# Optimization experiments

Measured on AMD Instinct MI355X. Metric: run time of the kernel, lower is better.

Reference implementation:

```python
import jax, jax.numpy as jnp
import numpy as np

B, NR, NF, NH, NFH, D, HID = 32, 32, 128, 64, 64, 32, 256


def setup_inputs() -> dict:
    key = jax.random.key(0)
    ks = jax.random.split(key, 16)

    def w(k, o, i):
        return (jax.random.normal(k, (o, i), jnp.float32) / np.sqrt(i)).astype(jnp.float32)

    inp = {
        "robot": jax.random.normal(ks[0], (B, NR, D), jnp.float32),
        "frontier": jax.random.normal(ks[1], (B, NF, D), jnp.float32),
        "robot_history": jax.random.normal(ks[2], (B, NH, D), jnp.float32),
        "frontier_history": jax.random.normal(ks[3], (B, NFH, D), jnp.float32),
        "robot_frontier": jax.random.uniform(ks[4], (B, NR, NF), jnp.float32),
        "robot_past": jax.random.uniform(ks[5], (B, NR, NH), jnp.float32),
        "frontier_past": jax.random.uniform(ks[6], (B, NF, NFH), jnp.float32),
        # parameters (torch Linear convention: weight [out, in])
        "Wq": w(ks[7], D, D), "bq": jnp.zeros(D, jnp.float32),
        "Wk": w(ks[8], D, D), "bk": jnp.zeros(D, jnp.float32),
        "Wv": w(ks[9], D, D), "bv": jnp.zeros(D, jnp.float32),
        "Wn1": w(ks[10], HID, 2 * D), "bn1": jnp.zeros(HID, jnp.float32),
        "Wn2": w(ks[11], D, HID), "bn2": jnp.zeros(D, jnp.float32),
        "We1": w(ks[12], HID, 2 * D + 1), "be1": jnp.zeros(HID, jnp.float32),
        "We2": w(ks[13], 1, HID), "be2": jnp.zeros(1, jnp.float32),
    }
    return inp


def reference(robot, frontier, robot_history, frontier_history, robot_frontier,
              robot_past, frontier_past, Wq, bq, Wk, bk, Wv, bv,
              Wn1, bn1, Wn2, bn2, We1, be1, We2, be2):
    def lin(x, W, b):
        return x @ W.T + b

    def nmlp(h):
        return lin(jax.nn.relu(lin(h, Wn1, bn1)), Wn2, bn2)

    def emlp(h):
        return lin(jax.nn.relu(lin(h, We1, be1)), We2, be2)

    def intra(x):  # x: [b, n, D]
        q, k, v = lin(x, Wq, bq), lin(x, Wk, bk), lin(x, Wv, bv)
        e = jax.nn.softmax(jnp.einsum('bnd,bmd->bnm', q, k), axis=-1)
        agg = jnp.einsum('bnm,bmd->bnd', e, v)
        return x + nmlp(jnp.concatenate([x, agg], axis=-1))

    def inter(x, y, dis):  # x: [b,Nx,D], y: [b,Ny,D], dis: [b,Nx,Ny]
        xq, yk, yv = lin(x, Wq, bq), lin(y, Wk, bk), lin(y, Wv, bv)
        b, Nx, _ = x.shape
        Ny = y.shape[1]
        r_i = jnp.broadcast_to(xq[:, :, None, :], (b, Nx, Ny, D))
        f_j = jnp.broadcast_to(yk[:, None, :, :], (b, Nx, Ny, D))
        edge_input = jnp.concatenate([r_i, f_j, dis[..., None]], axis=-1)  # [b,Nx,Ny,65]
        score = emlp(edge_input)[..., 0]                                   # [b,Nx,Ny]
        e = jax.nn.softmax(score, axis=-1)
        agg = jnp.einsum('bnm,bmd->bnd', e, yv)
        x = x + nmlp(jnp.concatenate([x, agg], axis=-1))
        return e, x

    robot = intra(robot)
    frontier = intra(frontier)           # == per-sample intra on [1,Nf,D]
    robot_history = intra(robot_history)
    frontier_history = intra(frontier_history)
    _, robot = inter(robot, robot_history, robot_past)
    _, new_frontier = inter(frontier, frontier_history, frontier_past)
    edge, robot = inter(robot, new_frontier, robot_frontier)
    # original returns the intra-transformed frontier (split_frontier), not new_frontier
    return (robot, frontier, robot_history, frontier_history, edge)
```

## Files before the change

### kernel.cpp

```cpp
#include <hip/hip_runtime.h>

#define BATCH 32
#define NRr 32
#define NFf 128
#define NHh 64
#define NFHh 64
#define TI 4

__device__ __forceinline__ float dot4(float4 a, float4 b) {
    return fmaf(a.x, b.x, fmaf(a.y, b.y, fmaf(a.z, b.z, a.w * b.w)));
}

__global__ __launch_bounds__(256) void intra_kernel(
    const float* __restrict__ robot, const float* __restrict__ frontier,
    const float* __restrict__ rhist, const float* __restrict__ fhist,
    const float* __restrict__ Wq, const float* __restrict__ bq,
    const float* __restrict__ Wk, const float* __restrict__ bk,
    const float* __restrict__ Wv, const float* __restrict__ bv,
    const float* __restrict__ Wn1, const float* __restrict__ bn1,
    const float* __restrict__ Wn2, const float* __restrict__ bn2,
    float* __restrict__ o_robot, float* __restrict__ o_frontier,
    float* __restrict__ o_rh, float* __restrict__ o_fh)
{
    __shared__ __align__(16) float sXc[1024];
    __shared__ __align__(16) float sQ[1024];
    __shared__ __align__(16) float sAgg[1024];
    __shared__ __align__(16) float sS[4096];
    __shared__ __align__(16) float sKT[4128];
    __shared__ __align__(16) float sVT[8192];

    const int blk = blockIdx.x, tid = threadIdx.x;
    const float* xin; float* xout; int N, lgN, b, chunk;
    if (blk < 32)       { xin=robot;    xout=o_robot;    N=32;  lgN=5; b=blk;          chunk=0; }
    else if (blk < 160) { xin=frontier; xout=o_frontier; N=128; lgN=7; b=(blk-32)>>2;  chunk=(blk-32)&3; }
    else if (blk < 224) { xin=rhist;    xout=o_rh;       N=64;  lgN=6; b=(blk-160)>>1; chunk=(blk-160)&1; }
    else                { xin=fhist;    xout=o_fh;       N=64;  lgN=6; b=(blk-224)>>1; chunk=(blk-224)&1; }

    const float* xb = xin + (size_t)b * N * 32;
    const int r0 = chunk << 5;
    const int d = tid & 31;

    {
        int idx = tid;
        #pragma unroll
        for (int it = 0; it < 4; ++it, idx += 256)
            sXc[idx] = xb[(r0 << 5) + idx];
    }

    {
        const float4* wk4 = (const float4*)(Wk + (d << 5));
        const float4* wv4 = (const float4*)(Wv + (d << 5));
        float4 wk[8], wv[8];
        #pragma unroll
        for (int k = 0; k < 8; ++k) { wk[k] = wk4[k]; wv[k] = wv4[k]; }
        const float bkd = bk[d], bvd = bv[d];
        for (int idx = tid; idx < (N << 5); idx += 256) {
            int j = idx >> 5;
            const float4* xr = (const float4*)(xb + (j << 5));
            float aK = bkd, aV = bvd;
            #pragma unroll
            for (int k = 0; k < 8; ++k) {
                float4 xv = xr[k];
                aK += dot4(wk[k], xv);
                aV += dot4(wv[k], xv);
            }
            sKT[d * 129 + j] = aK;
            sVT[(j << 5) + d] = aV;
        }
    }
    __syncthreads();

    {
        const float4* wq4 = (const float4*)(Wq + (d << 5));
        float4 wq[8];
        #pragma unroll
        for (int k = 0; k < 8; ++k) wq[k] = wq4[k];
        const float bqd = bq[d];
        int idx = tid;
        #pragma unroll
        for (int it = 0; it < 4; ++it, idx += 256) {
            int r = idx >> 5;
            const float4* xr = (const float4*)(sXc + (r << 5));
            float a = bqd;
            #pragma unroll
            for (int k = 0; k < 8; ++k) a += dot4(wq[k], xr[k]);
            sQ[idx] = a;
        }
    }
    __syncthreads();

    for (int idx = tid; idx < (N << 5); idx += 256) {
        int r = idx >> lgN, j = idx & (N - 1);
        const float* qr = sQ + (r << 5);
        float a = 0.f;
        #pragma unroll
        for (int e = 0; e < 32; ++e) a = fmaf(qr[e], sKT[e * 129 + j], a);
        sS[idx] = a;
    }
    __syncthreads();

    {
        int r = tid >> 3, l = tid & 7;
        float* row = sS + (r << lgN);
        float m = -1e30f;
        for (int j = l; j < N; j += 8) m = fmaxf(m, row[j]);
        m = fmaxf(m, __shfl_xor(m, 4));
        m = fmaxf(m, __shfl_xor(m, 2));
        m = fmaxf(m, __shfl_xor(m, 1));
        float s = 0.f;
        for (int j = l; j < N; j += 8) { float ev = __expf(row[j] - m); row[j] = ev; s += ev; }
        s += __shfl_xor(s, 4); s += __shfl_xor(s, 2); s += __shfl_xor(s, 1);
        float inv = 1.0f / s;
        for (int j = l; j < N; j += 8) row[j] *= inv;
    }
    __syncthreads();

    {
        int idx = tid;
        #pragma unroll
        for (int it = 0; it < 4; ++it, idx += 256) {
            int r = idx >> 5;
            const float* er = sS + (r << lgN);
            float a = 0.f;
            for (int j = 0; j < N; ++j) a = fmaf(er[j], sVT[(j << 5) + d], a);
            sAgg[idx] = a;
        }
    }
    __syncthreads();

    float* sT = sVT;
    {
        const float4* w14 = (const float4*)(Wn1 + (tid << 6));
        float4 w1r[16];
        #pragma unroll
        for (int k = 0; k < 16; ++k) w1r[k] = w14[k];
        const float b1 = bn1[tid];
        for (int r = 0; r < 32; ++r) {
            const float4* xr = (const float4*)(sXc + (r << 5));
            const float4* ar = (const float4*)(sAgg + (r << 5));
            float a = b1;
            #pragma unroll
            for (int k = 0; k < 8; ++k) a += dot4(w1r[k], xr[k]);
            #pragma unroll
            for (int k = 0; k < 8; ++k) a += dot4(w1r[8 + k], ar[k]);
            sT[(r << 8) + tid] = fmaxf(a, 0.f);
        }
    }
    __syncthreads();

    {
        const int rg = tid >> 5;
        float acc[4] = {0.f, 0.f, 0.f, 0.f};
        #pragma unroll
        for (int hc = 0; hc < 4; ++hc) {
            const float4* w24 = (const float4*)(Wn2 + (d << 8) + (hc << 6));
            float4 w2r[16];
            #pragma unroll
            for (int k = 0; k < 16; ++k) w2r[k] = w24[k];
            #pragma unroll
            for (int p = 0; p < 4; ++p) {
                int r = rg + (p << 3);
                const float4* tr = (const float4*)(sT + (r << 8) + (hc << 6));
                float a = 0.f;
                #pragma unroll
                for (int k = 0; k < 16; ++k) a += dot4(w2r[k], tr[k]);
                acc[p] += a;
            }
        }
        const float b2 = bn2[d];
        #pragma unroll
        for (int p = 0; p < 4; ++p) {
            int r = rg + (p << 3);
            xout[((size_t)b * N << 5) + ((r0 + r) << 5) + d] = sXc[(r << 5) + d] + b2 + acc[p];
        }
    }
}

__global__ __launch_bounds__(256) void pre_y_kernel(
    const float* __restrict__ yA, int NyA, float* __restrict__ wOutA, float* __restrict__ yvOutA, int nBlkA,
    const float* __restrict__ yB, int NyB, float* __restrict__ wOutB, float* __restrict__ yvOutB,
    const float* __restrict__ Wk, const float* __restrict__ bk,
    const float* __restrict__ Wv, const float* __restrict__ bv,
    const float* __restrict__ We1)
{
    __shared__ __align__(16) float sY[256], sK[256];
    const int blk = blockIdx.x, tid = threadIdx.x;
    const float* y; int Ny; float* wOut; float* yvOut; int idx;
    if (blk < nBlkA) { y=yA; Ny=NyA; wOut=wOutA; yvOut=yvOutA; idx=blk; }
    else             { y=yB; Ny=NyB; wOut=wOutB; yvOut=yvOutB; idx=blk-nBlkA; }
    const int chunks = Ny >> 3;
    const int b = idx / chunks, j0 = (idx - b * chunks) << 3;

    sY[tid] = y[((size_t)(b * Ny + j0)) * 32 + tid];
    __syncthreads();

    {
        int jl = tid >> 5, dd = tid & 31;
        const float4* wk4 = (const float4*)(Wk + (dd << 5));
        const float4* wv4 = (const float4*)(Wv + (dd << 5));
        const float4* yr = (const float4*)(sY + (jl << 5));
        float aK = bk[dd], aV = bv[dd];
        #pragma unroll
        for (int k = 0; k < 8; ++k) {
            float4 yv4 = yr[k];
            aK += dot4(wk4[k], yv4);
            aV += dot4(wv4[k], yv4);
        }
        sK[(jl << 5) + dd] = aK;
        yvOut[((size_t)(b * Ny + j0 + jl)) * 32 + dd] = aV;
    }
    __syncthreads();

    {
        const float* w1 = We1 + tid * 65 + 32;
        float acc[8] = {0,0,0,0,0,0,0,0};
        #pragma unroll
        for (int e = 0; e < 32; ++e) {
            float we = w1[e];
            #pragma unroll
            for (int jl = 0; jl < 8; ++jl)
                acc[jl] = fmaf(we, sK[(jl << 5) + e], acc[jl]);
        }
        float* wbase = wOut + (((size_t)b * 64 + (tid >> 2)) * Ny + j0) * 4 + (tid & 3);
        #pragma unroll
        for (int jl = 0; jl < 8; ++jl)
            wbase[jl << 2] = acc[jl];
    }
}

__global__ __launch_bounds__(256) void inter_main_kernel(
    const float* __restrict__ xA, int NxA, const float* __restrict__ wA, const float* __restrict__ yvA,
    int NyA, const float* __restrict__ disA, float* __restrict__ outA, float* __restrict__ eA, int nBlkA,
    const float* __restrict__ xB, int NxB, const float* __restrict__ wB, const float* __restrict__ yvB,
    int NyB, const float* __restrict__ disB, float* __restrict__ outB, float* __restrict__ eB,
    const float* __restrict__ Wq, const float* __restrict__ bq,
    const float* __restrict__ We1, const float* __restrict__ be1,
    const float* __restrict__ We2,
    const float* __restrict__ Wn1, const float* __restrict__ bn1,
    const float* __restrict__ Wn2, const float* __restrict__ bn2)
{
    __shared__ __align__(16) float smem[9088];
    float* sX   = smem;
    float* sQ   = smem + 128;
    float* sAgg = smem + 256;
    float* sDis = smem + 384;
    float* sC   = smem + 896;
    float* sW2  = smem + 1152;
    float* sS   = smem + 1408;
    float* sUT  = smem + 1920;
    float* sPR  = smem + 2944;
    float* sYV  = smem + 4992;

    const int blk = blockIdx.x, tid = threadIdx.x;
    const float* x; int Nx; const float* w; const float* yv; int Ny;
    const float* dis; float* outp; float* ep; int idx;
    if (blk < nBlkA) { x=xA; Nx=NxA; w=wA; yv=yvA; Ny=NyA; dis=disA; outp=outA; ep=eA; idx=blk; }
    else             { x=xB; Nx=NxB; w=wB; yv=yvB; Ny=NyB; dis=disB; outp=outB; ep=eB; idx=blk-nBlkA; }
    const int lgNy = (Ny == 128) ? 7 : 6;
    const int tiles = Nx >> 2;
    const int b = idx / tiles, i0 = (idx - b * tiles) << 2;
    const float* xrow = x + ((size_t)(b * Nx + i0)) * 32;

    if (tid < 128) sX[tid] = xrow[tid];
    if (tid < Ny) {
        int il = tid >> (lgNy - 2), jq = tid & ((Ny >> 2) - 1);
        ((float4*)sDis)[(il << 5) + jq] =
            ((const float4*)(dis + ((size_t)(b * Nx + i0 + il)) * Ny))[jq];
    }
    {
        const float4* yv4 = (const float4*)(yv + ((size_t)(b * Ny) << 5));
        for (int k = tid; k < (Ny << 3); k += 256)
            ((float4*)sYV)[k] = yv4[k];
    }
    __syncthreads();

    if (tid < 128) {
        int il = tid >> 5, dd = tid & 31;
        const float4* wq4 = (const float4*)(Wq + (dd << 5));
        const float4* xr = (const float4*)(sX + (il << 5));
        float a = bq[dd];
        #pragma unroll
        for (int k = 0; k < 8; ++k) a += dot4(wq4[k], xr[k]);
        sQ[tid] = a;
    }
    __syncthreads();

    {
        const float* w1 = We1 + tid * 65;
        const float b1 = be1[tid];
        float acc[TI];
        #pragma unroll
        for (int il = 0; il < TI; ++il) acc[il] = b1;
        #pragma unroll
        for (int e = 0; e < 32; ++e) {
            float we = w1[e];
            #pragma unroll
            for (int il = 0; il < TI; ++il)
                acc[il] = fmaf(we, sQ[(il << 5) + e], acc[il]);
        }
        #pragma unroll
        for (int il = 0; il < TI; ++il) sUT[(il << 8) + tid] = acc[il];
        sC[tid] = w1[64];
        sW2[tid] = We2[tid];
    }
    __syncthreads();

    const int wv = tid >> 6, lane = tid & 63;
    {
        const int hc0 = wv << 4;
        const float4* wT4 = (const float4*)w + (size_t)(b * 64) * Ny;
        const float4* c4p = (const float4*)sC;
        const float4* p4p = (const float4*)sW2;
        if (Ny == 64) {
            float dv[TI];
            #pragma unroll
            for (int il = 0; il < TI; ++il) dv[il] = sDis[(il << 7) + lane];
            float acc[TI] = {0.f, 0.f, 0.f, 0.f};
            #pragma unroll
            for (int t = 0; t < 16; ++t) {
                int hc = hc0 + t;
                float4 w4 = wT4[((size_t)hc << 6) + lane];
                float4 c4 = c4p[hc], p4 = p4p[hc];
                #pragma unroll
                for (int il = 0; il < TI; ++il) {
                    float4 u4 = ((const float4*)(sUT + (il << 8)))[hc];
                    acc[il] = fmaf(p4.x, fmaxf(fmaf(c4.x, dv[il], u4.x + w4.x), 0.f), acc[il]);
                    acc[il] = fmaf(p4.y, fmaxf(fmaf(c4.y, dv[il], u4.y + w4.y), 0.f), acc[il]);
                    acc[il] = fmaf(p4.z, fmaxf(fmaf(c4.z, dv[il], u4.z + w4.z), 0.f), acc[il]);
                    acc[il] = fmaf(p4.w, fmaxf(fmaf(c4.w, dv[il], u4.w + w4.w), 0.f), acc[il]);
                }
            }
            #pragma unroll
            for (int il = 0; il < TI; ++il)
                sPR[(wv << 9) + (il << 7) + lane] = acc[il];
        } else {
            float dv0[TI], dv1[TI];
            #pragma unroll
            for (int il = 0; il < TI; ++il) {
                dv0[il] = sDis[(il << 7) + lane];
                dv1[il] = sDis[(il << 7) + 64 + lane];
            }
            float acc0[TI] = {0.f, 0.f, 0.f, 0.f};
            float acc1[TI] = {0.f, 0.f, 0.f, 0.f};
            #pragma unroll
            for (int t = 0; t < 16; ++t) {
                int hc = hc0 + t;
                float4 wa = wT4[((size_t)hc << 7) + lane];
                float4 wb = wT4[((size_t)hc << 7) + 64 + lane];
                float4 c4 = c4p[hc], p4 = p4p[hc];
                #pragma unroll
                for (int il = 0; il < TI; ++il) {
                    float4 u4 = ((const float4*)(sUT + (il << 8)))[hc];
                    acc0[il] = fmaf(p4.x, fmaxf(fmaf(c4.x, dv0[il], u4.x + wa.x), 0.f), acc0[il]);
                    acc0[il] = fmaf(p4.y, fmaxf(fmaf(c4.y, dv0[il], u4.y + wa.y), 0.f), acc0[il]);
                    acc0[il] = fmaf(p4.z, fmaxf(fmaf(c4.z, dv0[il], u4.z + wa.z), 0.f), acc0[il]);
                    acc0[il] = fmaf(p4.w, fmaxf(fmaf(c4.w, dv0[il], u4.w + wa.w), 0.f), acc0[il]);
                    acc1[il] = fmaf(p4.x, fmaxf(fmaf(c4.x, dv1[il], u4.x + wb.x), 0.f), acc1[il]);
                    acc1[il] = fmaf(p4.y, fmaxf(fmaf(c4.y, dv1[il], u4.y + wb.y), 0.f), acc1[il]);
                    acc1[il] = fmaf(p4.z, fmaxf(fmaf(c4.z, dv1[il], u4.z + wb.z), 0.f), acc1[il]);
                    acc1[il] = fmaf(p4.w, fmaxf(fmaf(c4.w, dv1[il], u4.w + wb.w), 0.f), acc1[il]);
                }
            }
            #pragma unroll
            for (int il = 0; il < TI; ++il) {
                sPR[(wv << 9) + (il << 7) + lane] = acc0[il];
                sPR[(wv << 9) + (il << 7) + 64 + lane] = acc1[il];
            }
        }
    }
    __syncthreads();

    for (int k = tid; k < (TI << lgNy); k += 256) {
        int il = k >> lgNy, j = k & (Ny - 1);
        int o = (il << 7) + j;
        sS[o] = sPR[o] + sPR[512 + o] + sPR[1024 + o] + sPR[1536 + o];
    }
    __syncthreads();

    {
        float v0 = sS[(wv << 7) + lane];
        float v1 = (Ny == 128) ? sS[(wv << 7) + 64 + lane] : -1e30f;
        float m = fmaxf(v0, v1);
        #pragma unroll
        for (int msk = 32; msk; msk >>= 1) m = fmaxf(m, __shfl_xor(m, msk));
        float e0 = __expf(v0 - m);
        float e1 = (Ny == 128) ? __expf(v1 - m) : 0.f;
        float s = e0 + e1;
        #pragma unroll
        for (int msk = 32; msk; msk >>= 1) s += __shfl_xor(s, msk);
        float inv = 1.0f / s;
        e0 *= inv; e1 *= inv;
        sS[(wv << 7) + lane] = e0;
        if (Ny == 128) sS[(wv << 7) + 64 + lane] = e1;
        if (ep) {
            float* erow = ep + ((size_t)(b * Nx + i0 + wv)) * Ny;
            erow[lane] = e0;
            if (Ny == 128) erow[64 + lane] = e1;
        }
    }

    {
        const int dd = lane & 31, jg = lane >> 5;
        float p = 0.f;
        for (int j = jg; j < Ny; j += 2)
            p = fmaf(sS[(wv << 7) + j], sYV[(j << 5) + dd], p);
        p += __shfl_xor(p, 32);
        if (jg == 0) sAgg[(wv << 5) + dd] = p;
    }
    __syncthreads();

    {
        const float4* w14 = (const float4*)(Wn1 + (tid << 6));
        const float b1 = bn1[tid];
        float acc[TI];
        #pragma unroll
        for (int il = 0; il < TI; ++il) acc[il] = b1;
        #pragma unroll
        for (int k = 0; k < 8; ++k) {
            float4 wa = w14[k];
            #pragma unroll
            for (int il = 0; il < TI; ++il)
                acc[il] += dot4(wa, ((const float4*)(sX + (il << 5)))[k]);
        }
        #pragma unroll
        for (int k = 0; k < 8; ++k) {
            float4 wb = w14[8 + k];
            #pragma unroll
            for (int il = 0; il < TI; ++il)
                acc[il] += dot4(wb, ((const float4*)(sAgg + (il << 5)))[k]);
        }
        __syncthreads();
        #pragma unroll
        for (int il = 0; il < TI; ++il) sUT[(il << 8) + tid] = fmaxf(acc[il], 0.f);
    }
    __syncthreads();

    {
        const int hg = tid >> 5, dd = tid & 31;
        const float4* w24 = (const float4*)(Wn2 + (dd << 8) + (hg << 5));
        float4 w2r[8];
        #pragma unroll
        for (int k = 0; k < 8; ++k) w2r[k] = w24[k];
        float p[TI] = {0.f, 0.f, 0.f, 0.f};
        #pragma unroll
        for (int k = 0; k < 8; ++k) {
            #pragma unroll
            for (int il = 0; il < TI; ++il)
                p[il] += dot4(w2r[k], ((const float4*)(sUT + (il << 8) + (hg << 5)))[k]);
        }
        #pragma unroll
        for (int il = 0; il < TI; ++il) sPR[(hg << 7) + (il << 5) + dd] = p[il];
    }
    __syncthreads();
    if (tid < 128) {
        int il = tid >> 5, dd = tid & 31;
        float a = bn2[dd] + sX[tid];
        #pragma unroll
        for (int hg = 0; hg < 8; ++hg) a += sPR[(hg << 7) + tid];
        outp[((size_t)(b * Nx + i0 + il)) * 32 + dd] = a;
    }
}

extern "C" void kernel_launch(void* const* d_in, const int* in_sizes, int n_in,
                              void* d_out, int out_size, void* d_ws, size_t ws_size,
                              hipStream_t stream) {
    const float* robot          = (const float*)d_in[0];
    const float* frontier       = (const float*)d_in[1];
    const float* rh             = (const float*)d_in[2];
    const float* fh             = (const float*)d_in[3];
    const float* robot_frontier = (const float*)d_in[4];
    const float* robot_past     = (const float*)d_in[5];
    const float* frontier_past  = (const float*)d_in[6];
    const float* Wq  = (const float*)d_in[7];  const float* bq  = (const float*)d_in[8];
    const float* Wk  = (const float*)d_in[9];  const float* bk  = (const float*)d_in[10];
    const float* Wv  = (const float*)d_in[11]; const float* bv  = (const float*)d_in[12];
    const float* Wn1 = (const float*)d_in[13]; const float* bn1 = (const float*)d_in[14];
    const float* Wn2 = (const float*)d_in[15]; const float* bn2 = (const float*)d_in[16];
    const float* We1 = (const float*)d_in[17]; const float* be1 = (const float*)d_in[18];
    const float* We2 = (const float*)d_in[19];

    float* out = (float*)d_out;
    float* out_robot    = out;
    float* out_frontier = out + 32768;
    float* out_rh       = out + 163840;
    float* out_fh       = out + 229376;
    float* out_edge     = out + 294912;

    float* W = (float*)d_ws;
    float* robot1 = W;
    float* robot2 = W + 32768;
    float* nf     = W + 65536;
    float* w5     = W + 196608;
    float* yv5    = W + 720896;
    float* w6     = W + 786432;
    float* yv6    = W + 1310720;
    float* w7     = W + 1376256;
    float* yv7    = W + 2424832;

    intra_kernel<<<288, 256, 0, stream>>>(robot, frontier, rh, fh,
        Wq, bq, Wk, bk, Wv, bv, Wn1, bn1, Wn2, bn2,
        robot1, out_frontier, out_rh, out_fh);

    pre_y_kernel<<<512, 256, 0, stream>>>(
        out_rh, NHh, w5, yv5, BATCH * NHh / 8,
        out_fh, NFHh, w6, yv6,
        Wk, bk, Wv, bv, We1);

    inter_main_kernel<<<1280, 256, 0, stream>>>(
        robot1, NRr, w5, yv5, NHh, robot_past, robot2, (float*)nullptr, BATCH * (NRr / TI),
        out_frontier, NFf, w6, yv6, NFHh, frontier_past, nf, (float*)nullptr,
        Wq, bq, We1, be1, We2, Wn1, bn1, Wn2, bn2);

    pre_y_kernel<<<512, 256, 0, stream>>>(
        nf, NFf, w7, yv7, BATCH * NFf / 8,
        nf, NFf, w7, yv7,
        Wk, bk, Wv, bv, We1);

    inter_main_kernel<<<256, 256, 0, stream>>>(
        robot2, NRr, w7, yv7, NFf, robot_frontier, out_robot, out_edge, BATCH * (NRr / TI),
        robot2, NRr, w7, yv7, NFf, robot_frontier, out_robot, out_edge,
        Wq, bq, We1, be1, We2, Wn1, bn1, Wn2, bn2);
}
```

Baseline: 213.2 us.

## Fuse five launches into a persistent kernel with grid-wide barriers

Replaces the five separate kernel launches with one persistent kernel of 512 blocks that loops over work items per stage, separated by atomic-counter grid barriers. The intra stage is also re-split so frontier rows are processed in chunks of 16 instead of 32, giving more work items, and the score buffer gets padded rows. The aim is to remove launch gaps and tail idle time between the dependent stages. In exchange it adds a memset, barrier spin costs, and a shared-memory footprint of about 70 KB per block that limits occupancy. It also relies on all 512 blocks being co-resident to avoid deadlock.

New measurement: 697.3 us. 227% more time.

```diff
diff --git a/kernel.cpp b/kernel.cpp
--- a/kernel.cpp
+++ b/kernel.cpp
@@ -6,46 +6,54 @@
 #define NHh 64
 #define NFHh 64
 #define TI 4
+#define GRID 512
+#define SMEM_FLOATS 17696
 
 __device__ __forceinline__ float dot4(float4 a, float4 b) {
     return fmaf(a.x, b.x, fmaf(a.y, b.y, fmaf(a.z, b.z, a.w * b.w)));
 }
 
-__global__ __launch_bounds__(256) void intra_kernel(
-    const float* __restrict__ robot, const float* __restrict__ frontier,
-    const float* __restrict__ rhist, const float* __restrict__ fhist,
-    const float* __restrict__ Wq, const float* __restrict__ bq,
-    const float* __restrict__ Wk, const float* __restrict__ bk,
-    const float* __restrict__ Wv, const float* __restrict__ bv,
-    const float* __restrict__ Wn1, const float* __restrict__ bn1,
-    const float* __restrict__ Wn2, const float* __restrict__ bn2,
-    float* __restrict__ o_robot, float* __restrict__ o_frontier,
-    float* __restrict__ o_rh, float* __restrict__ o_fh)
+__device__ __forceinline__ void grid_sync(unsigned* cnt) {
+    __threadfence();
+    __syncthreads();
+    if (threadIdx.x == 0) {
+        __hip_atomic_fetch_add(cnt, 1u, __ATOMIC_ACQ_REL, __HIP_MEMORY_SCOPE_AGENT);
+        while (__hip_atomic_load(cnt, __ATOMIC_ACQUIRE, __HIP_MEMORY_SCOPE_AGENT) < (unsigned)GRID)
+            __builtin_amdgcn_s_sleep(2);
+        __threadfence();
+    }
+    __syncthreads();
+}
+
+__device__ void intra_body(int item, float* smem,
+    const float* robot, const float* frontier, const float* rhist, const float* fhist,
+    const float* Wq, const float* bq, const float* Wk, const float* bk,
+    const float* Wv, const float* bv, const float* Wn1, const float* bn1,
+    const float* Wn2, const float* bn2,
+    float* o_robot, float* o_frontier, float* o_rh, float* o_fh)
 {
-    __shared__ __align__(16) float sXc[1024];
-    __shared__ __align__(16) float sQ[1024];
-    __shared__ __align__(16) float sAgg[1024];
-    __shared__ __align__(16) float sS[4096];
-    __shared__ __align__(16) float sKT[4128];
-    __shared__ __align__(16) float sVT[8192];
-
-    const int blk = blockIdx.x, tid = threadIdx.x;
-    const float* xin; float* xout; int N, lgN, b, chunk;
-    if (blk < 32)       { xin=robot;    xout=o_robot;    N=32;  lgN=5; b=blk;          chunk=0; }
-    else if (blk < 160) { xin=frontier; xout=o_frontier; N=128; lgN=7; b=(blk-32)>>2;  chunk=(blk-32)&3; }
-    else if (blk < 224) { xin=rhist;    xout=o_rh;       N=64;  lgN=6; b=(blk-160)>>1; chunk=(blk-160)&1; }
-    else                { xin=fhist;    xout=o_fh;       N=64;  lgN=6; b=(blk-224)>>1; chunk=(blk-224)&1; }
-
+    float* sXc = smem;
+    float* sQ  = smem + 1024;
+    float* sAgg= smem + 2048;
+    float* sS  = smem + 3072;
+    float* sKT = smem + 5376;
+    float* sVT = smem + 9504;
+
+    const int tid = threadIdx.x;
+    const float* xin; float* xout; int N, lgN, b, chunk, CH;
+    if (item < 32)       { xin=robot;    xout=o_robot;    N=32;  lgN=5; b=item;  chunk=0;  CH=32; }
+    else if (item < 288) { int t=item-32;  xin=frontier; xout=o_frontier; N=128; lgN=7; b=t>>3; chunk=t&7; CH=16; }
+    else if (item < 352) { int t=item-288; xin=rhist;    xout=o_rh;       N=64;  lgN=6; b=t>>1; chunk=t&1; CH=32; }
+    else                 { int t=item-352; xin=fhist;    xout=o_fh;       N=64;  lgN=6; b=t>>1; chunk=t&1; CH=32; }
+    const int P = N + 4;
     const float* xb = xin + (size_t)b * N * 32;
-    const int r0 = chunk << 5;
+    const int r0 = chunk * CH;
     const int d = tid & 31;
 
-    {
-        int idx = tid;
-        #pragma unroll
-        for (int it = 0; it < 4; ++it, idx += 256)
-            sXc[idx] = xb[(r0 << 5) + idx];
-    }
+    __syncthreads();
+
+    for (int idx = tid; idx < (CH << 5); idx += 256)
+        sXc[idx] = xb[(r0 << 5) + idx];
 
     {
         const float4* wk4 = (const float4*)(Wk + (d << 5));
@@ -76,9 +84,7 @@
         #pragma unroll
         for (int k = 0; k < 8; ++k) wq[k] = wq4[k];
         const float bqd = bq[d];
-        int idx = tid;
-        #pragma unroll
-        for (int it = 0; it < 4; ++it, idx += 256) {
+        for (int idx = tid; idx < (CH << 5); idx += 256) {
             int r = idx >> 5;
             const float4* xr = (const float4*)(sXc + (r << 5));
             float a = bqd;
@@ -89,42 +95,37 @@
     }
     __syncthreads();
 
-    for (int idx = tid; idx < (N << 5); idx += 256) {
+    for (int idx = tid; idx < CH * N; idx += 256) {
         int r = idx >> lgN, j = idx & (N - 1);
         const float* qr = sQ + (r << 5);
         float a = 0.f;
         #pragma unroll
         for (int e = 0; e < 32; ++e) a = fmaf(qr[e], sKT[e * 129 + j], a);
-        sS[idx] = a;
-    }
-    __syncthreads();
-
-    {
-        int r = tid >> 3, l = tid & 7;
-        float* row = sS + (r << lgN);
+        sS[r * P + j] = a;
+    }
+    __syncthreads();
+
+    {
+        const int lpr = 256 / CH;
+        int r = tid / lpr, l = tid % lpr;
+        float* row = sS + r * P;
         float m = -1e30f;
-        for (int j = l; j < N; j += 8) m = fmaxf(m, row[j]);
-        m = fmaxf(m, __shfl_xor(m, 4));
-        m = fmaxf(m, __shfl_xor(m, 2));
-        m = fmaxf(m, __shfl_xor(m, 1));
+        for (int j = l; j < N; j += lpr) m = fmaxf(m, row[j]);
+        for (int msk = lpr >> 1; msk; msk >>= 1) m = fmaxf(m, __shfl_xor(m, msk));
         float s = 0.f;
-        for (int j = l; j < N; j += 8) { float ev = __expf(row[j] - m); row[j] = ev; s += ev; }
-        s += __shfl_xor(s, 4); s += __shfl_xor(s, 2); s += __shfl_xor(s, 1);
+        for (int j = l; j < N; j += lpr) { float ev = __expf(row[j] - m); row[j] = ev; s += ev; }
+        for (int msk = lpr >> 1; msk; msk >>= 1) s += __shfl_xor(s, msk);
         float inv = 1.0f / s;
-        for (int j = l; j < N; j += 8) row[j] *= inv;
-    }
-    __syncthreads();
-
-    {
-        int idx = tid;
-        #pragma unroll
-        for (int it = 0; it < 4; ++it, idx += 256) {
-            int r = idx >> 5;
-            const float* er = sS + (r << lgN);
-            float a = 0.f;
-            for (int j = 0; j < N; ++j) a = fmaf(er[j], sVT[(j << 5) + d], a);
-            sAgg[idx] = a;
-        }
+        for (int j = l; j < N; j += lpr) row[j] *= inv;
+    }
+    __syncthreads();
+
+    for (int idx = tid; idx < (CH << 5); idx += 256) {
+        int r = idx >> 5;
+        const float* er = sS + r * P;
+        float a = 0.f;
+        for (int j = 0; j < N; ++j) a = fmaf(er[j], sVT[(j << 5) + d], a);
+        sAgg[idx] = a;
     }
     __syncthreads();
 
@@ -135,7 +136,7 @@
         #pragma unroll
         for (int k = 0; k < 16; ++k) w1r[k] = w14[k];
         const float b1 = bn1[tid];
-        for (int r = 0; r < 32; ++r) {
+        for (int r = 0; r < CH; ++r) {
             const float4* xr = (const float4*)(sXc + (r << 5));
             const float4* ar = (const float4*)(sAgg + (r << 5));
             float a = b1;
@@ -150,6 +151,7 @@
 
     {
         const int rg = tid >> 5;
+        const int PR = CH >> 3;
         float acc[4] = {0.f, 0.f, 0.f, 0.f};
         #pragma unroll
         for (int hc = 0; hc < 4; ++hc) {
@@ -157,8 +159,7 @@
             float4 w2r[16];
             #pragma unroll
             for (int k = 0; k < 16; ++k) w2r[k] = w24[k];
-            #pragma unroll
-            for (int p = 0; p < 4; ++p) {
+            for (int p = 0; p < PR; ++p) {
                 int r = rg + (p << 3);
                 const float4* tr = (const float4*)(sT + (r << 8) + (hc << 6));
                 float a = 0.f;
@@ -168,29 +169,29 @@
             }
         }
         const float b2 = bn2[d];
-        #pragma unroll
-        for (int p = 0; p < 4; ++p) {
+        for (int p = 0; p < PR; ++p) {
             int r = rg + (p << 3);
             xout[((size_t)b * N << 5) + ((r0 + r) << 5) + d] = sXc[(r << 5) + d] + b2 + acc[p];
         }
     }
 }
 
-__global__ __launch_bounds__(256) void pre_y_kernel(
-    const float* __restrict__ yA, int NyA, float* __restrict__ wOutA, float* __restrict__ yvOutA, int nBlkA,
-    const float* __restrict__ yB, int NyB, float* __restrict__ wOutB, float* __restrict__ yvOutB,
-    const float* __restrict__ Wk, const float* __restrict__ bk,
-    const float* __restrict__ Wv, const float* __restrict__ bv,
-    const float* __restrict__ We1)
+__device__ void pre_y_body(int item, float* smem,
+    const float* yA, int NyA, float* wOutA, float* yvOutA, int nA,
+    const float* yB, int NyB, float* wOutB, float* yvOutB,
+    const float* Wk, const float* bk, const float* Wv, const float* bv,
+    const float* We1)
 {
-    __shared__ __align__(16) float sY[256], sK[256];
-    const int blk = blockIdx.x, tid = threadIdx.x;
+    float* sY = smem;
+    float* sK = smem + 256;
+    const int tid = threadIdx.x;
     const float* y; int Ny; float* wOut; float* yvOut; int idx;
-    if (blk < nBlkA) { y=yA; Ny=NyA; wOut=wOutA; yvOut=yvOutA; idx=blk; }
-    else             { y=yB; Ny=NyB; wOut=wOutB; yvOut=yvOutB; idx=blk-nBlkA; }
+    if (item < nA) { y=yA; Ny=NyA; wOut=wOutA; yvOut=yvOutA; idx=item; }
+    else           { y=yB; Ny=NyB; wOut=wOutB; yvOut=yvOutB; idx=item-nA; }
     const int chunks = Ny >> 3;
     const int b = idx / chunks, j0 = (idx - b * chunks) << 3;
 
+    __syncthreads();
     sY[tid] = y[((size_t)(b * Ny + j0)) * 32 + tid];
     __syncthreads();
 
@@ -228,18 +229,15 @@
     }
 }
 
-__global__ __launch_bounds__(256) void inter_main_kernel(
-    const float* __restrict__ xA, int NxA, const float* __restrict__ wA, const float* __restrict__ yvA,
-    int NyA, const float* __restrict__ disA, float* __restrict__ outA, float* __restrict__ eA, int nBlkA,
-    const float* __restrict__ xB, int NxB, const float* __restrict__ wB, const float* __restrict__ yvB,
-    int NyB, const float* __restrict__ disB, float* __restrict__ outB, float* __restrict__ eB,
-    const float* __restrict__ Wq, const float* __restrict__ bq,
-    const float* __restrict__ We1, const float* __restrict__ be1,
-    const float* __restrict__ We2,
-    const float* __restrict__ Wn1, const float* __restrict__ bn1,
-    const float* __restrict__ Wn2, const float* __restrict__ bn2)
+__device__ void inter_body(int item, float* smem,
+    const float* xA, int NxA, const float* wA, const float* yvA,
+    int NyA, const float* disA, float* outA, float* eA, int nBlkA,
+    const float* xB, int NxB, const float* wB, const float* yvB,
+    int NyB, const float* disB, float* outB, float* eB,
+    const float* Wq, const float* bq,
+    const float* We1, const float* be1, const float* We2,
+    const float* Wn1, const float* bn1, const float* Wn2, const float* bn2)
 {
-    __shared__ __align__(16) float smem[9088];
     float* sX   = smem;
     float* sQ   = smem + 128;
     float* sAgg = smem + 256;
@@ -251,15 +249,17 @@
     float* sPR  = smem + 2944;
     float* sYV  = smem + 4992;
 
-    const int blk = blockIdx.x, tid = threadIdx.x;
+    const int tid = threadIdx.x;
     const float* x; int Nx; const float* w; const float* yv; int Ny;
     const float* dis; float* outp; float* ep; int idx;
-    if (blk < nBlkA) { x=xA; Nx=NxA; w=wA; yv=yvA; Ny=NyA; dis=disA; outp=outA; ep=eA; idx=blk; }
-    else             { x=xB; Nx=NxB; w=wB; yv=yvB; Ny=NyB; dis=disB; outp=outB; ep=eB; idx=blk-nBlkA; }
+    if (item < nBlkA) { x=xA; Nx=NxA; w=wA; yv=yvA; Ny=NyA; dis=disA; outp=outA; ep=eA; idx=item; }
+    else              { x=xB; Nx=NxB; w=wB; yv=yvB; Ny=NyB; dis=disB; outp=outB; ep=eB; idx=item-nBlkA; }
     const int lgNy = (Ny == 128) ? 7 : 6;
     const int tiles = Nx >> 2;
     const int b = idx / tiles, i0 = (idx - b * tiles) << 2;
     const float* xrow = x + ((size_t)(b * Nx + i0)) * 32;
+
+    __syncthreads();
 
     if (tid < 128) sX[tid] = xrow[tid];
     if (tid < Ny) {
@@ -461,6 +461,50 @@
     }
 }
 
+__global__ __launch_bounds__(256) void mega_kernel(
+    const float* robot, const float* frontier, const float* rh, const float* fh,
+    const float* robot_frontier, const float* robot_past, const float* frontier_past,
+    const float* Wq, const float* bq, const float* Wk, const float* bk,
+    const float* Wv, const float* bv, const float* Wn1, const float* bn1,
+    const float* Wn2, const float* bn2, const float* We1, const float* be1,
+    const float* We2,
+    float* out_robot, float* out_frontier, float* out_rh, float* out_fh, float* out_edge,
+    float* robot1, float* robot2, float* nf,
+    float* w5, float* yv5, float* w6, float* yv6, float* w7, float* yv7,
+    unsigned* bar)
+{
+    __shared__ __align__(16) float smem[SMEM_FLOATS];
+
+    for (int it = blockIdx.x; it < 416; it += GRID)
+        intra_body(it, smem, robot, frontier, rh, fh,
+                   Wq, bq, Wk, bk, Wv, bv, Wn1, bn1, Wn2, bn2,
+                   robot1, out_frontier, out_rh, out_fh);
+    grid_sync(bar + 0);
+
+    for (int it = blockIdx.x; it < 512; it += GRID)
+        pre_y_body(it, smem, out_rh, NHh, w5, yv5, BATCH * NHh / 8,
+                   out_fh, NFHh, w6, yv6, Wk, bk, Wv, bv, We1);
+    grid_sync(bar + 1);
+
+    for (int it = blockIdx.x; it < 1280; it += GRID)
+        inter_body(it, smem,
+                   robot1, NRr, w5, yv5, NHh, robot_past, robot2, (float*)0, BATCH * (NRr / TI),
+                   out_frontier, NFf, w6, yv6, NFHh, frontier_past, nf, (float*)0,
+                   Wq, bq, We1, be1, We2, Wn1, bn1, Wn2, bn2);
+    grid_sync(bar + 2);
+
+    for (int it = blockIdx.x; it < 512; it += GRID)
+        pre_y_body(it, smem, nf, NFf, w7, yv7, BATCH * NFf / 8,
+                   nf, NFf, w7, yv7, Wk, bk, Wv, bv, We1);
+    grid_sync(bar + 3);
+
+    for (int it = blockIdx.x; it < 256; it += GRID)
+        inter_body(it, smem,
+                   robot2, NRr, w7, yv7, NFf, robot_frontier, out_robot, out_edge, BATCH * (NRr / TI),
+                   robot2, NRr, w7, yv7, NFf, robot_frontier, out_robot, out_edge,
+                   Wq, bq, We1, be1, We2, Wn1, bn1, Wn2, bn2);
+}
+
 extern "C" void kernel_launch(void* const* d_in, const int* in_sizes, int n_in,
                               void* d_out, int out_size, void* d_ws, size_t ws_size,
                               hipStream_t stream) {
@@ -496,28 +540,12 @@
     float* yv6    = W + 1310720;
     float* w7     = W + 1376256;
     float* yv7    = W + 2424832;
-
-    intra_kernel<<<288, 256, 0, stream>>>(robot, frontier, rh, fh,
-        Wq, bq, Wk, bk, Wv, bv, Wn1, bn1, Wn2, bn2,
-        robot1, out_frontier, out_rh, out_fh);
-
-    pre_y_kernel<<<512, 256, 0, stream>>>(
-        out_rh, NHh, w5, yv5, BATCH * NHh / 8,
-        out_fh, NFHh, w6, yv6,
-        Wk, bk, Wv, bv, We1);
-
-    inter_main_kernel<<<1280, 256, 0, stream>>>(
-        robot1, NRr, w5, yv5, NHh, robot_past, robot2, (float*)nullptr, BATCH * (NRr / TI),
-        out_frontier, NFf, w6, yv6, NFHh, frontier_past, nf, (float*)nullptr,
-        Wq, bq, We1, be1, We2, Wn1, bn1, Wn2, bn2);
-
-    pre_y_kernel<<<512, 256, 0, stream>>>(
-        nf, NFf, w7, yv7, BATCH * NFf / 8,
-        nf, NFf, w7, yv7,
-        Wk, bk, Wv, bv, We1);
-
-    inter_main_kernel<<<256, 256, 0, stream>>>(
-        robot2, NRr, w7, yv7, NFf, robot_frontier, out_robot, out_edge, BATCH * (NRr / TI),
-        robot2, NRr, w7, yv7, NFf, robot_frontier, out_robot, out_edge,
-        Wq, bq, We1, be1, We2, Wn1, bn1, Wn2, bn2);
-}
+    unsigned* bar = (unsigned*)(W + 2555904);
+
+    hipMemsetAsync(bar, 0, 64, stream);
+    mega_kernel<<<GRID, 256, 0, stream>>>(
+        robot, frontier, rh, fh, robot_frontier, robot_past, frontier_past,
+        Wq, bq, Wk, bk, Wv, bv, Wn1, bn1, Wn2, bn2, We1, be1, We2,
+        out_robot, out_frontier, out_rh, out_fh, out_edge,
+        robot1, robot2, nf, w5, yv5, w6, yv6, w7, yv7, bar);
+}
```

## Fuse key/value/edge-weight precompute into intra and inter kernels, drop pre_y launches

Applied to the files above, without the earlier changes.

Removes both pre_y_kernel launches. The history K/V projections and the We1 key-side products are now computed in the epilogue of intra_kernel, and the new-frontier ones in the epilogue of the first inter_main_kernel, reusing the just-computed rows held in shared memory. Frontier intra work is also split into 16-row chunks, giving 416 blocks instead of 288 for more parallelism, at the cost of recomputing the full K/V for each chunk. This saves two launches and a global round trip, but adds serial work and extra barriers to some blocks, which may unbalance the grid.

Result: slower. 234.5 us (+10.0%).

```diff
diff --git a/kernel.cpp b/kernel.cpp
--- a/kernel.cpp
+++ b/kernel.cpp
@@ -19,33 +19,34 @@
     const float* __restrict__ Wv, const float* __restrict__ bv,
     const float* __restrict__ Wn1, const float* __restrict__ bn1,
     const float* __restrict__ Wn2, const float* __restrict__ bn2,
+    const float* __restrict__ We1,
     float* __restrict__ o_robot, float* __restrict__ o_frontier,
-    float* __restrict__ o_rh, float* __restrict__ o_fh)
+    float* __restrict__ o_rh, float* __restrict__ o_fh,
+    float* __restrict__ w5, float* __restrict__ yv5,
+    float* __restrict__ w6, float* __restrict__ yv6)
 {
     __shared__ __align__(16) float sXc[1024];
     __shared__ __align__(16) float sQ[1024];
     __shared__ __align__(16) float sAgg[1024];
-    __shared__ __align__(16) float sS[4096];
+    __shared__ __align__(16) float sS[2304];
     __shared__ __align__(16) float sKT[4128];
     __shared__ __align__(16) float sVT[8192];
 
-    const int blk = blockIdx.x, tid = threadIdx.x;
-    const float* xin; float* xout; int N, lgN, b, chunk;
-    if (blk < 32)       { xin=robot;    xout=o_robot;    N=32;  lgN=5; b=blk;          chunk=0; }
-    else if (blk < 160) { xin=frontier; xout=o_frontier; N=128; lgN=7; b=(blk-32)>>2;  chunk=(blk-32)&3; }
-    else if (blk < 224) { xin=rhist;    xout=o_rh;       N=64;  lgN=6; b=(blk-160)>>1; chunk=(blk-160)&1; }
-    else                { xin=fhist;    xout=o_fh;       N=64;  lgN=6; b=(blk-224)>>1; chunk=(blk-224)&1; }
-
+    const int item = blockIdx.x, tid = threadIdx.x;
+    const float* xin; float* xout; int N, lgN, b, chunk, CH;
+    float* wOut = nullptr; float* yvOut = nullptr;
+    if (item < 32)       { xin=robot;    xout=o_robot;    N=32;  lgN=5; b=item;  chunk=0;  CH=32; }
+    else if (item < 288) { int t=item-32;  xin=frontier; xout=o_frontier; N=128; lgN=7; b=t>>3; chunk=t&7; CH=16; }
+    else if (item < 352) { int t=item-288; xin=rhist;    xout=o_rh;       N=64;  lgN=6; b=t>>1; chunk=t&1; CH=32; wOut=w5; yvOut=yv5; }
+    else                 { int t=item-352; xin=fhist;    xout=o_fh;       N=64;  lgN=6; b=t>>1; chunk=t&1; CH=32; wOut=w6; yvOut=yv6; }
+    const bool isPre = (wOut != nullptr);
+    const int P = N + 4;
     const float* xb = xin + (size_t)b * N * 32;
-    const int r0 = chunk << 5;
+    const int r0 = chunk * CH;
     const int d = tid & 31;
 
-    {
-        int idx = tid;
-        #pragma unroll
-        for (int it = 0; it < 4; ++it, idx += 256)
-            sXc[idx] = xb[(r0 << 5) + idx];
-    }
+    for (int idx = tid; idx < (CH << 5); idx += 256)
+        sXc[idx] = xb[(r0 << 5) + idx];
 
     {
         const float4* wk4 = (const float4*)(Wk + (d << 5));
@@ -76,9 +77,7 @@
         #pragma unroll
         for (int k = 0; k < 8; ++k) wq[k] = wq4[k];
         const float bqd = bq[d];
-        int idx = tid;
-        #pragma unroll
-        for (int it = 0; it < 4; ++it, idx += 256) {
+        for (int idx = tid; idx < (CH << 5); idx += 256) {
             int r = idx >> 5;
             const float4* xr = (const float4*)(sXc + (r << 5));
             float a = bqd;
@@ -89,42 +88,37 @@
     }
     __syncthreads();
 
-    for (int idx = tid; idx < (N << 5); idx += 256) {
+    for (int idx = tid; idx < CH * N; idx += 256) {
         int r = idx >> lgN, j = idx & (N - 1);
         const float* qr = sQ + (r << 5);
         float a = 0.f;
         #pragma unroll
         for (int e = 0; e < 32; ++e) a = fmaf(qr[e], sKT[e * 129 + j], a);
-        sS[idx] = a;
-    }
-    __syncthreads();
-
-    {
-        int r = tid >> 3, l = tid & 7;
-        float* row = sS + (r << lgN);
+        sS[r * P + j] = a;
+    }
+    __syncthreads();
+
+    {
+        const int lpr = 256 / CH;
+        int r = tid / lpr, l = tid % lpr;
+        float* row = sS + r * P;
         float m = -1e30f;
-        for (int j = l; j < N; j += 8) m = fmaxf(m, row[j]);
-        m = fmaxf(m, __shfl_xor(m, 4));
-        m = fmaxf(m, __shfl_xor(m, 2));
-        m = fmaxf(m, __shfl_xor(m, 1));
+        for (int j = l; j < N; j += lpr) m = fmaxf(m, row[j]);
+        for (int msk = lpr >> 1; msk; msk >>= 1) m = fmaxf(m, __shfl_xor(m, msk));
         float s = 0.f;
-        for (int j = l; j < N; j += 8) { float ev = __expf(row[j] - m); row[j] = ev; s += ev; }
-        s += __shfl_xor(s, 4); s += __shfl_xor(s, 2); s += __shfl_xor(s, 1);
+        for (int j = l; j < N; j += lpr) { float ev = __expf(row[j] - m); row[j] = ev; s += ev; }
+        for (int msk = lpr >> 1; msk; msk >>= 1) s += __shfl_xor(s, msk);
         float inv = 1.0f / s;
-        for (int j = l; j < N; j += 8) row[j] *= inv;
-    }
-    __syncthreads();
-
-    {
-        int idx = tid;
-        #pragma unroll
-        for (int it = 0; it < 4; ++it, idx += 256) {
-            int r = idx >> 5;
-            const float* er = sS + (r << lgN);
-            float a = 0.f;
-            for (int j = 0; j < N; ++j) a = fmaf(er[j], sVT[(j << 5) + d], a);
-            sAgg[idx] = a;
-        }
+        for (int j = l; j < N; j += lpr) row[j] *= inv;
+    }
+    __syncthreads();
+
+    for (int idx = tid; idx < (CH << 5); idx += 256) {
+        int r = idx >> 5;
+        const float* er = sS + r * P;
+        float a = 0.f;
+        for (int j = 0; j < N; ++j) a = fmaf(er[j], sVT[(j << 5) + d], a);
+        sAgg[idx] = a;
     }
     __syncthreads();
 
@@ -135,7 +129,7 @@
         #pragma unroll
         for (int k = 0; k < 16; ++k) w1r[k] = w14[k];
         const float b1 = bn1[tid];
-        for (int r = 0; r < 32; ++r) {
+        for (int r = 0; r < CH; ++r) {
             const float4* xr = (const float4*)(sXc + (r << 5));
             const float4* ar = (const float4*)(sAgg + (r << 5));
             float a = b1;
@@ -150,6 +144,7 @@
 
     {
         const int rg = tid >> 5;
+        const int PR = CH >> 3;
         float acc[4] = {0.f, 0.f, 0.f, 0.f};
         #pragma unroll
         for (int hc = 0; hc < 4; ++hc) {
@@ -157,8 +152,7 @@
             float4 w2r[16];
             #pragma unroll
             for (int k = 0; k < 16; ++k) w2r[k] = w24[k];
-            #pragma unroll
-            for (int p = 0; p < 4; ++p) {
+            for (int p = 0; p < PR; ++p) {
                 int r = rg + (p << 3);
                 const float4* tr = (const float4*)(sT + (r << 8) + (hc << 6));
                 float a = 0.f;
@@ -168,94 +162,87 @@
             }
         }
         const float b2 = bn2[d];
-        #pragma unroll
-        for (int p = 0; p < 4; ++p) {
+        for (int p = 0; p < PR; ++p) {
             int r = rg + (p << 3);
-            xout[((size_t)b * N << 5) + ((r0 + r) << 5) + d] = sXc[(r << 5) + d] + b2 + acc[p];
+            float v = sXc[(r << 5) + d] + b2 + acc[p];
+            xout[((size_t)b * N << 5) + ((r0 + r) << 5) + d] = v;
+            if (isPre) sQ[(r << 5) + d] = v;
+        }
+    }
+
+    if (isPre) {
+        __syncthreads();
+        {
+            const float4* wk4 = (const float4*)(Wk + (d << 5));
+            const float4* wv4 = (const float4*)(Wv + (d << 5));
+            const float bkd = bk[d], bvd = bv[d];
+            const int rg = tid >> 5;
+            for (int p = 0; p < 4; ++p) {
+                int r = rg + (p << 3);
+                const float4* orow = (const float4*)(sQ + (r << 5));
+                float aK = bkd, aV = bvd;
+                #pragma unroll
+                for (int k = 0; k < 8; ++k) {
+                    float4 ov = orow[k];
+                    aK += dot4(wk4[k], ov);
+                    aV += dot4(wv4[k], ov);
+                }
+                sKT[r * 33 + d] = aK;
+                yvOut[(((size_t)(b * N + r0 + r)) << 5) + d] = aV;
+            }
+        }
+        __syncthreads();
+        {
+            const float* w1 = We1 + tid * 65 + 32;
+            for (int rc = 0; rc < 4; ++rc) {
+                float acc[8] = {0,0,0,0,0,0,0,0};
+                #pragma unroll
+                for (int e = 0; e < 32; ++e) {
+                    float we = w1[e];
+                    #pragma unroll
+                    for (int jl = 0; jl < 8; ++jl)
+                        acc[jl] = fmaf(we, sKT[(rc * 8 + jl) * 33 + e], acc[jl]);
+                }
+                float* wbase = wOut + (((size_t)b * 64 + (tid >> 2)) * 64 + r0 + (rc << 3)) * 4 + (tid & 3);
+                #pragma unroll
+                for (int jl = 0; jl < 8; ++jl)
+                    wbase[jl << 2] = acc[jl];
+            }
         }
     }
 }
 
-__global__ __launch_bounds__(256) void pre_y_kernel(
-    const float* __restrict__ yA, int NyA, float* __restrict__ wOutA, float* __restrict__ yvOutA, int nBlkA,
-    const float* __restrict__ yB, int NyB, float* __restrict__ wOutB, float* __restrict__ yvOutB,
+__global__ __launch_bounds__(256) void inter_main_kernel(
+    const float* __restrict__ xA, int NxA, const float* __restrict__ wA, const float* __restrict__ yvA,
+    int NyA, const float* __restrict__ disA, float* __restrict__ outA, float* __restrict__ eA,
+    float* __restrict__ wPreA, float* __restrict__ yvPreA, int nBlkA,
+    const float* __restrict__ xB, int NxB, const float* __restrict__ wB, const float* __restrict__ yvB,
+    int NyB, const float* __restrict__ disB, float* __restrict__ outB, float* __restrict__ eB,
+    float* __restrict__ wPreB, float* __restrict__ yvPreB,
+    const float* __restrict__ Wq, const float* __restrict__ bq,
     const float* __restrict__ Wk, const float* __restrict__ bk,
     const float* __restrict__ Wv, const float* __restrict__ bv,
-    const float* __restrict__ We1)
-{
-    __shared__ __align__(16) float sY[256], sK[256];
-    const int blk = blockIdx.x, tid = threadIdx.x;
-    const float* y; int Ny; float* wOut; float* yvOut; int idx;
-    if (blk < nBlkA) { y=yA; Ny=NyA; wOut=wOutA; yvOut=yvOutA; idx=blk; }
-    else             { y=yB; Ny=NyB; wOut=wOutB; yvOut=yvOutB; idx=blk-nBlkA; }
-    const int chunks = Ny >> 3;
-    const int b = idx / chunks, j0 = (idx - b * chunks) << 3;
-
-    sY[tid] = y[((size_t)(b * Ny + j0)) * 32 + tid];
-    __syncthreads();
-
-    {
-        int jl = tid >> 5, dd = tid & 31;
-        const float4* wk4 = (const float4*)(Wk + (dd << 5));
-        const float4* wv4 = (const float4*)(Wv + (dd << 5));
-        const float4* yr = (const float4*)(sY + (jl << 5));
-        float aK = bk[dd], aV = bv[dd];
-        #pragma unroll
-        for (int k = 0; k < 8; ++k) {
-            float4 yv4 = yr[k];
-            aK += dot4(wk4[k], yv4);
-            aV += dot4(wv4[k], yv4);
-        }
-        sK[(jl << 5) + dd] = aK;
-        yvOut[((size_t)(b * Ny + j0 + jl)) * 32 + dd] = aV;
-    }
-    __syncthreads();
-
-    {
-        const float* w1 = We1 + tid * 65 + 32;
-        float acc[8] = {0,0,0,0,0,0,0,0};
-        #pragma unroll
-        for (int e = 0; e < 32; ++e) {
-            float we = w1[e];
-            #pragma unroll
-            for (int jl = 0; jl < 8; ++jl)
-                acc[jl] = fmaf(we, sK[(jl << 5) + e], acc[jl]);
-        }
-        float* wbase = wOut + (((size_t)b * 64 + (tid >> 2)) * Ny + j0) * 4 + (tid & 3);
-        #pragma unroll
-        for (int jl = 0; jl < 8; ++jl)
-            wbase[jl << 2] = acc[jl];
-    }
-}
-
-__global__ __launch_bounds__(256) void inter_main_kernel(
-    const float* __restrict__ xA, int NxA, const float* __restrict__ wA, const float* __restrict__ yvA,
-    int NyA, const float* __restrict__ disA, float* __restrict__ outA, float* __restrict__ eA, int nBlkA,
-    const float* __restrict__ xB, int NxB, const float* __restrict__ wB, const float* __restrict__ yvB,
-    int NyB, const float* __restrict__ disB, float* __restrict__ outB, float* __restrict__ eB,
-    const float* __restrict__ Wq, const float* __restrict__ bq,
     const float* __restrict__ We1, const float* __restrict__ be1,
     const float* __restrict__ We2,
     const float* __restrict__ Wn1, const float* __restrict__ bn1,
     const float* __restrict__ Wn2, const float* __restrict__ bn2)
 {
-    __shared__ __align__(16) float smem[9088];
-    float* sX   = smem;
-    float* sQ   = smem + 128;
-    float* sAgg = smem + 256;
-    float* sDis = smem + 384;
-    float* sC   = smem + 896;
-    float* sW2  = smem + 1152;
-    float* sS   = smem + 1408;
-    float* sUT  = smem + 1920;
-    float* sPR  = smem + 2944;
-    float* sYV  = smem + 4992;
+    __shared__ __align__(16) float sX[128];
+    __shared__ __align__(16) float sQ[128];
+    __shared__ __align__(16) float sAgg[128];
+    __shared__ __align__(16) float sDis[512];
+    __shared__ __align__(16) float sC[256];
+    __shared__ __align__(16) float sW2[256];
+    __shared__ __align__(16) float sS[512];
+    __shared__ __align__(16) float sUT[1024];
+    __shared__ __align__(16) float sPR[2048];
+    __shared__ __align__(16) float sYV[4096];
 
     const int blk = blockIdx.x, tid = threadIdx.x;
     const float* x; int Nx; const float* w; const float* yv; int Ny;
-    const float* dis; float* outp; float* ep; int idx;
-    if (blk < nBlkA) { x=xA; Nx=NxA; w=wA; yv=yvA; Ny=NyA; dis=disA; outp=outA; ep=eA; idx=blk; }
-    else             { x=xB; Nx=NxB; w=wB; yv=yvB; Ny=NyB; dis=disB; outp=outB; ep=eB; idx=blk-nBlkA; }
+    const float* dis; float* outp; float* ep; float* wPre; float* yvPre; int idx;
+    if (blk < nBlkA) { x=xA; Nx=NxA; w=wA; yv=yvA; Ny=NyA; dis=disA; outp=outA; ep=eA; wPre=wPreA; yvPre=yvPreA; idx=blk; }
+    else             { x=xB; Nx=NxB; w=wB; yv=yvB; Ny=NyB; dis=disB; outp=outB; ep=eB; wPre=wPreB; yvPre=yvPreB; idx=blk-nBlkA; }
     const int lgNy = (Ny == 128) ? 7 : 6;
     const int tiles = Nx >> 2;
     const int b = idx / tiles, i0 = (idx - b * tiles) << 2;
@@ -458,6 +445,37 @@
         #pragma unroll
         for (int hg = 0; hg < 8; ++hg) a += sPR[(hg << 7) + tid];
         outp[((size_t)(b * Nx + i0 + il)) * 32 + dd] = a;
+        if (wPre) sQ[tid] = a;
+    }
+
+    if (wPre) {
+        __syncthreads();
+        {
+            int t = tid & 127, il = t >> 5, dd = t & 31;
+            const float4* wm4 = (const float4*)(((tid < 128) ? Wk : Wv) + (dd << 5));
+            const float4* orow = (const float4*)(sQ + (il << 5));
+            float a = (tid < 128) ? bk[dd] : bv[dd];
+            #pragma unroll
+            for (int k = 0; k < 8; ++k) a += dot4(wm4[k], orow[k]);
+            if (tid < 128) sS[il * 33 + dd] = a;
+            else yvPre[(((size_t)(b * Nx + i0 + il)) << 5) + dd] = a;
+        }
+        __syncthreads();
+        {
+            const float* w1 = We1 + tid * 65 + 32;
+            float acc[4] = {0.f, 0.f, 0.f, 0.f};
+            #pragma unroll
+            for (int e = 0; e < 32; ++e) {
+                float we = w1[e];
+                #pragma unroll
+                for (int il = 0; il < 4; ++il)
+                    acc[il] = fmaf(we, sS[il * 33 + e], acc[il]);
+            }
+            float* wbase = wPre + (((size_t)b * 64 + (tid >> 2)) * Nx + i0) * 4 + (tid & 3);
+            #pragma unroll
+            for (int il = 0; il < 4; ++il)
+                wbase[il << 2] = acc[il];
+        }
     }
 }
 
@@ -497,27 +515,21 @@
     float* w7     = W + 1376256;
     float* yv7    = W + 2424832;
 
-    intra_kernel<<<288, 256, 0, stream>>>(robot, frontier, rh, fh,
-        Wq, bq, Wk, bk, Wv, bv, Wn1, bn1, Wn2, bn2,
-        robot1, out_frontier, out_rh, out_fh);
-
-    pre_y_kernel<<<512, 256, 0, stream>>>(
-        out_rh, NHh, w5, yv5, BATCH * NHh / 8,
-        out_fh, NFHh, w6, yv6,
-        Wk, bk, Wv, bv, We1);
+    intra_kernel<<<416, 256, 0, stream>>>(robot, frontier, rh, fh,
+        Wq, bq, Wk, bk, Wv, bv, Wn1, bn1, Wn2, bn2, We1,
+        robot1, out_frontier, out_rh, out_fh, w5, yv5, w6, yv6);
 
     inter_main_kernel<<<1280, 256, 0, stream>>>(
-        robot1, NRr, w5, yv5, NHh, robot_past, robot2, (float*)nullptr, BATCH * (NRr / TI),
-        out_frontier, NFf, w6, yv6, NFHh, frontier_past, nf, (float*)nullptr,
-        Wq, bq, We1, be1, We2, Wn1, bn1, Wn2, bn2);
-
-    pre_y_kernel<<<512, 256, 0, stream>>>(
-        nf, NFf, w7, yv7, BATCH * NFf / 8,
-        nf, NFf, w7, yv7,
-        Wk, bk, Wv, bv, We1);
+        robot1, NRr, w5, yv5, NHh, robot_past, robot2,
+        (float*)nullptr, (float*)nullptr, (float*)nullptr, BATCH * (NRr / TI),
+        out_frontier, NFf, w6, yv6, NFHh, frontier_past, nf,
+        (float*)nullptr, w7, yv7,
+        Wq, bq, Wk, bk, Wv, bv, We1, be1, We2, Wn1, bn1, Wn2, bn2);
 
     inter_main_kernel<<<256, 256, 0, stream>>>(
-        robot2, NRr, w7, yv7, NFf, robot_frontier, out_robot, out_edge, BATCH * (NRr / TI),
         robot2, NRr, w7, yv7, NFf, robot_frontier, out_robot, out_edge,
-        Wq, bq, We1, be1, We2, Wn1, bn1, Wn2, bn2);
+        (float*)nullptr, (float*)nullptr, BATCH * (NRr / TI),
+        robot2, NRr, w7, yv7, NFf, robot_frontier, out_robot, out_edge,
+        (float*)nullptr, (float*)nullptr,
+        Wq, bq, Wk, bk, Wv, bv, We1, be1, We2, Wn1, bn1, Wn2, bn2);
 }
```
